# Kernel optimization log

Measured on AMD Instinct MI355X. Metric: run time of the kernel, lower is better.

The kernel has to match this reference:

```python
import jax, jax.numpy as jnp
import numpy as np
import math

D_MODEL = 1024
N_HEADS = 16
D_HEAD = D_MODEL // N_HEADS
WINDOW_LEN = 128
DILATION = 4
SEQ = 3072
BATCH = 1


def setup_inputs() -> dict:
    key = jax.random.key(0)
    ks = jax.random.split(key, 10)
    def xavier(k, shape):
        fan_out, fan_in = shape
        lim = math.sqrt(6.0 / (fan_in + fan_out))
        return jax.random.uniform(k, shape, jnp.float32, -lim, lim)
    return {
        "x": jax.random.normal(ks[0], (SEQ, BATCH, D_MODEL), jnp.float32),
        "beta": 0.1 * jax.random.normal(ks[1], (N_HEADS,), jnp.float32),
        "Wq": xavier(ks[2], (D_MODEL, D_MODEL)),
        "bq": jnp.zeros((D_MODEL,), jnp.float32),
        "Wk": xavier(ks[3], (D_MODEL, D_MODEL)),
        "bk": jnp.zeros((D_MODEL,), jnp.float32),
        "Wv": xavier(ks[4], (D_MODEL, D_MODEL)),
        "bv": jnp.zeros((D_MODEL,), jnp.float32),
        "Wo": xavier(ks[5], (D_MODEL, D_MODEL)),
        "bo": jnp.zeros((D_MODEL,), jnp.float32),
    }


def _causal_windowed_bias(seq_len):
    # allowed iff 0 <= (i-j), (i-j)//dilation < window_len, (i-j) % dilation == 0
    idx = jnp.arange(seq_len)
    diff = idx[:, None] - idx[None, :]
    allowed = (diff >= 0) & (diff // DILATION < WINDOW_LEN) & (diff % DILATION == 0)
    return jnp.where(allowed, 0.0, -jnp.inf).astype(jnp.float32)  # [S, S]


def reference(x, beta, Wq, bq, Wk, bk, Wv, bv, Wo, bo):
    s, b, d = x.shape
    # projections: nn.Linear => x @ W.T + b
    def split_heads(t):  # [s, b, h*dh] -> [b, h, s, dh]
        return t.reshape(s, b, N_HEADS, D_HEAD).transpose(1, 2, 0, 3)
    q = split_heads(x @ Wq.T + bq)
    k = split_heads(x @ Wk.T + bk)
    v = split_heads(x @ Wv.T + bv)
    # beta scaling folded into q, attention uses scale=1.0
    q = q / (math.sqrt(D_HEAD) * jnp.exp(beta)[None, :, None, None])
    bias = _causal_windowed_bias(s)  # [S, S]
    scores = jnp.einsum('bhsd,bhtd->bhst', q, k) + bias
    attn = jax.nn.softmax(scores, axis=-1)
    ctx = jnp.einsum('bhst,bhtd->bhsd', attn, v)  # [b, h, s, dh]
    ctx = ctx.transpose(2, 0, 1, 3).reshape(s, b, d)  # [s, b, d_model]
    return ctx @ Wo.T + bo
```

## Files before the change

### kernel.cpp

```cpp
#include <hip/hip_runtime.h>
#include <math.h>

#define SEQ   3072
#define DM    1024
#define NH    16
#define DH    64
#define WIN   128
#define DIL   4
#define TSUB  768

typedef __attribute__((ext_vector_type(8))) short    short8;
typedef __attribute__((ext_vector_type(8))) _Float16 half8;
typedef __attribute__((ext_vector_type(4))) float    floatx4;

__device__ __forceinline__ float bf2f(unsigned short u) {
    return __uint_as_float(((unsigned)u) << 16);
}
__device__ __forceinline__ unsigned short f2bf(float f) {
    unsigned u = __float_as_uint(f);
    return (unsigned short)((u + 0x7FFFu + ((u >> 16) & 1u)) >> 16);
}
__device__ __forceinline__ unsigned short f2h(float f) {
    _Float16 h = (_Float16)f;
    return __builtin_bit_cast(unsigned short, h);
}

__device__ __forceinline__ void gload_lds16(const void* g, void* l) {
    __builtin_amdgcn_global_load_lds(
        (const __attribute__((address_space(1))) void*)g,
        (__attribute__((address_space(3))) void*)l, 16, 0, 0);
}

__global__ __launch_bounds__(256) void convert_kernel(
    const float* __restrict__ x,  const float* __restrict__ Wq,
    const float* __restrict__ Wk, const float* __restrict__ Wv,
    const float* __restrict__ Wo,
    ushort* __restrict__ xb,  ushort* __restrict__ Wqb,
    ushort* __restrict__ Wkb, ushort* __restrict__ Wvb,
    ushort* __restrict__ Wob)
{
    const float* s; ushort* d; int n;
    switch (blockIdx.y) {
        case 0: s = x;  d = xb;  n = SEQ * DM; break;
        case 1: s = Wq; d = Wqb; n = DM * DM;  break;
        case 2: s = Wk; d = Wkb; n = DM * DM;  break;
        case 3: s = Wv; d = Wvb; n = DM * DM;  break;
        default: s = Wo; d = Wob; n = DM * DM; break;
    }
    int i = (blockIdx.x * 256 + threadIdx.x) * 4;
    if (i >= n) return;
    float4 v = *(const float4*)&s[i];
    ushort4 o = { f2bf(v.x), f2bf(v.y), f2bf(v.z), f2bf(v.w) };
    *(ushort4*)&d[i] = o;
}

struct QkvSmem {
    ushort As[2][128][64];
    ushort Bs[2][64][64];
};

template<bool QSCALE>
__device__ __forceinline__ void gemm_qkv_body(QkvSmem& sm,
                                              const ushort* __restrict__ A,
                                              const ushort* __restrict__ W,
                                              const float* __restrict__ bias,
                                              const float* __restrict__ beta,
                                              ushort* __restrict__ C,
                                              int bx, int by)
{
    const int tid  = threadIdx.x;
    const int lane = tid & 63, w = tid >> 6;
    const int ln15 = lane & 15, quad = lane >> 4;
    const int wm = w >> 1, wn = w & 1;

    const int rl = lane >> 3, cl = lane & 7;
    const ushort* aRow[4];
#pragma unroll
    for (int i = 0; i < 4; ++i) {
        int row   = w * 32 + 8 * i + rl;
        int chunk = cl ^ ((row >> 1) & 7);
        aRow[i] = A + (size_t)(by * 128 + row) * DM + chunk * 8;
    }
    const ushort* bRow[2];
#pragma unroll
    for (int i = 0; i < 2; ++i) {
        int row   = w * 16 + 8 * i + rl;
        int chunk = cl ^ ((row >> 1) & 7);
        bRow[i] = W + (size_t)(bx * 64 + row) * DM + chunk * 8;
    }

    const floatx4 zero = {0.f, 0.f, 0.f, 0.f};
    floatx4 acc[4][2];
#pragma unroll
    for (int i = 0; i < 4; ++i)
#pragma unroll
        for (int j = 0; j < 2; ++j) acc[i][j] = zero;

#pragma unroll
    for (int i = 0; i < 4; ++i) gload_lds16(aRow[i], &sm.As[0][w * 32 + 8 * i][0]);
#pragma unroll
    for (int i = 0; i < 2; ++i) gload_lds16(bRow[i], &sm.Bs[0][w * 16 + 8 * i][0]);
    __syncthreads();

    const int rf = (ln15 >> 1) & 7;
#pragma unroll 2
    for (int t = 0; t < 16; ++t) {
        const int cur = t & 1, nxt = cur ^ 1;
        if (t < 15) {
            const int ko = (t + 1) * 64;
#pragma unroll
            for (int i = 0; i < 4; ++i) gload_lds16(aRow[i] + ko, &sm.As[nxt][w * 32 + 8 * i][0]);
#pragma unroll
            for (int i = 0; i < 2; ++i) gload_lds16(bRow[i] + ko, &sm.Bs[nxt][w * 16 + 8 * i][0]);
        }
#pragma unroll
        for (int s = 0; s < 2; ++s) {
            short8 af[4], bf[2];
#pragma unroll
            for (int i = 0; i < 4; ++i)
                af[i] = *(const short8*)&sm.As[cur][wm * 64 + i * 16 + ln15][((s * 4 + quad) ^ rf) * 8];
#pragma unroll
            for (int j = 0; j < 2; ++j)
                bf[j] = *(const short8*)&sm.Bs[cur][wn * 32 + j * 16 + ln15][((s * 4 + quad) ^ rf) * 8];
#pragma unroll
            for (int i = 0; i < 4; ++i)
#pragma unroll
                for (int j = 0; j < 2; ++j)
                    acc[i][j] = __builtin_amdgcn_mfma_f32_16x16x32_bf16(af[i], bf[j], acc[i][j], 0, 0, 0);
        }
        __syncthreads();
    }

#pragma unroll
    for (int j = 0; j < 2; ++j) {
        const int col = bx * 64 + wn * 32 + j * 16 + ln15;
        const float b = bias[col];
        const float scale = QSCALE ? 0.125f * __expf(-beta[col >> 6]) : 1.0f;
#pragma unroll
        for (int i = 0; i < 4; ++i) {
            const int row0 = by * 128 + wm * 64 + i * 16 + quad * 4;
#pragma unroll
            for (int rg = 0; rg < 4; ++rg) {
                float vv = (acc[i][j][rg] + b) * scale;
                C[(size_t)(row0 + rg) * DM + col] = f2bf(vv);
            }
        }
    }
}

__global__ __launch_bounds__(256, 3) void qkv_kernel(
    const ushort* __restrict__ xb,
    const ushort* __restrict__ Wqb, const float* __restrict__ bq,
    const ushort* __restrict__ Wkb, const float* __restrict__ bk,
    const ushort* __restrict__ Wvb, const float* __restrict__ bv,
    const float* __restrict__ beta,
    ushort* __restrict__ q, ushort* __restrict__ k, ushort* __restrict__ v)
{
    __shared__ QkvSmem sm;
    const int z = blockIdx.z;
    const ushort* W = (z == 0) ? Wqb : (z == 1) ? Wkb : Wvb;
    const float*  b = (z == 0) ? bq  : (z == 1) ? bk  : bv;
    ushort*       C = (z == 0) ? q   : (z == 1) ? k   : v;
    if (z == 0)
        gemm_qkv_body<true >(sm, xb, W, b, beta, C, blockIdx.x, blockIdx.y);
    else
        gemm_qkv_body<false>(sm, xb, W, b, nullptr, C, blockIdx.x, blockIdx.y);
}

__global__ __launch_bounds__(256, 3) void out_kernel(
    const ushort* __restrict__ ctxb, const ushort* __restrict__ Wob,
    const float* __restrict__ bo, float* __restrict__ out)
{
    __shared__ ushort As[2][64][64];
    __shared__ ushort Bs[2][64][64];

    const int tid  = threadIdx.x;
    const int lane = tid & 63, w = tid >> 6;
    const int ln15 = lane & 15, quad = lane >> 4;
    const int wm = w >> 1, wn = w & 1;
    const int bx = blockIdx.x, by = blockIdx.y;

    const int rl = lane >> 3, cl = lane & 7;
    const ushort* aRow[2]; const ushort* bRow[2];
#pragma unroll
    for (int i = 0; i < 2; ++i) {
        int row   = w * 16 + 8 * i + rl;
        int chunk = cl ^ ((row >> 1) & 7);
        aRow[i] = ctxb + (size_t)(by * 64 + row) * DM + chunk * 8;
        bRow[i] = Wob  + (size_t)(bx * 64 + row) * DM + chunk * 8;
    }

    const floatx4 zero = {0.f, 0.f, 0.f, 0.f};
    floatx4 acc[2][2];
#pragma unroll
    for (int i = 0; i < 2; ++i)
#pragma unroll
        for (int j = 0; j < 2; ++j) acc[i][j] = zero;

#pragma unroll
    for (int i = 0; i < 2; ++i) {
        gload_lds16(aRow[i], &As[0][w * 16 + 8 * i][0]);
        gload_lds16(bRow[i], &Bs[0][w * 16 + 8 * i][0]);
    }
    __syncthreads();

    const int rf = (ln15 >> 1) & 7;
#pragma unroll 2
    for (int t = 0; t < 16; ++t) {
        const int cur = t & 1, nxt = cur ^ 1;
        if (t < 15) {
            const int ko = (t + 1) * 64;
#pragma unroll
            for (int i = 0; i < 2; ++i) {
                gload_lds16(aRow[i] + ko, &As[nxt][w * 16 + 8 * i][0]);
                gload_lds16(bRow[i] + ko, &Bs[nxt][w * 16 + 8 * i][0]);
            }
        }
#pragma unroll
        for (int s = 0; s < 2; ++s) {
            short8 af[2], bf[2];
#pragma unroll
            for (int i = 0; i < 2; ++i)
                af[i] = *(const short8*)&As[cur][wm * 32 + i * 16 + ln15][((s * 4 + quad) ^ rf) * 8];
#pragma unroll
            for (int j = 0; j < 2; ++j)
                bf[j] = *(const short8*)&Bs[cur][wn * 32 + j * 16 + ln15][((s * 4 + quad) ^ rf) * 8];
#pragma unroll
            for (int i = 0; i < 2; ++i)
#pragma unroll
                for (int j = 0; j < 2; ++j)
                    acc[i][j] = __builtin_amdgcn_mfma_f32_16x16x32_bf16(af[i], bf[j], acc[i][j], 0, 0, 0);
        }
        __syncthreads();
    }

#pragma unroll
    for (int j = 0; j < 2; ++j) {
        const int col = bx * 64 + wn * 32 + j * 16 + ln15;
        const float b = bo[col];
#pragma unroll
        for (int i = 0; i < 2; ++i) {
            const int row0 = by * 64 + wm * 32 + i * 16 + quad * 4;
#pragma unroll
            for (int rg = 0; rg < 4; ++rg)
                out[(size_t)(row0 + rg) * DM + col] = acc[i][j][rg] + b;
        }
    }
}

struct AttnSmem {
    union {
        ushort Ks[192 * 64];
        ushort Vt[6 * 4 * 64 * 8];
    } u;
    float S[32][195];
    float Rsum[32];
};

__global__ __launch_bounds__(256) void attn_kernel(
    const ushort* __restrict__ q, const ushort* __restrict__ k,
    const ushort* __restrict__ v, ushort* __restrict__ ctx)
{
    __shared__ AttnSmem sm;

    const int tid  = threadIdx.x;
    const int lane = tid & 63, w = tid >> 6;
    const int ln15 = lane & 15, quad = lane >> 4;
    const int t0   = blockIdx.x * 32;
    const int r    = blockIdx.y;
    const int h    = blockIdx.z;
    const int hoff = h * DH;

    {
        const int kr = lane >> 3;
        const int swz = ((lane & 7) ^ kr) * 8;
#pragma unroll
        for (int ci = w * 6; ci < w * 6 + 6; ++ci) {
            int key = ci * 8 + kr;
            long grow = 4L * (t0 - 160 + key) + r;
            gload_lds16(k + grow * DM + hoff + swz, &sm.u.Ks[ci * 512]);
        }
    }

    const int qt = w >> 1;
    short8 qf0, qf1;
    {
        int qrow = qt * 16 + ln15;
        const ushort* gq = q + (4L * (t0 + qrow) + r) * DM + hoff + quad * 8;
        qf0 = *(const short8*)gq;
        qf1 = *(const short8*)(gq + 32);
    }

    short8 vreg[6];
#pragma unroll
    for (int it = 0; it < 6; ++it) {
        int idx = it * 256 + tid;
        int key = idx >> 3, d0 = (idx & 7) * 8;
        long grow = 4L * (t0 - 160 + key) + r;
        vreg[it] = *(const short8*)(v + grow * DM + hoff + d0);
    }

    __syncthreads();

    {
        const floatx4 zero = {0.f, 0.f, 0.f, 0.f};
        const int kt0 = (w & 1) * 6;
        const int lb  = ln15 & 7;
#pragma unroll
        for (int kk2 = 0; kk2 < 6; ++kk2) {
            const int kt  = kt0 + kk2;
            const int key = kt * 16 + ln15;
            short8 b0 = *(const short8*)&sm.u.Ks[key * 64 + ((quad ^ lb) << 3)];
            short8 b1 = *(const short8*)&sm.u.Ks[key * 64 + (((4 + quad) ^ lb) << 3)];
            floatx4 acc = zero;
            acc = __builtin_amdgcn_mfma_f32_16x16x32_bf16(qf0, b0, acc, 0, 0, 0);
            acc = __builtin_amdgcn_mfma_f32_16x16x32_bf16(qf1, b1, acc, 0, 0, 0);
            const int tp = t0 - 160 + key;
#pragma unroll
            for (int rg = 0; rg < 4; ++rg) {
                int qrow = qt * 16 + quad * 4 + rg;
                int tq = t0 + qrow;
                bool ok = (tp >= 0) && (tp <= tq) && (tp > tq - WIN);
                sm.S[qrow][key] = ok ? acc[rg] : -1e30f;
            }
        }
    }

    __syncthreads();

#pragma unroll
    for (int it = 0; it < 6; ++it) {
        int idx = it * 256 + tid;
        int key = idx >> 3, d0 = (idx & 7) * 8;
        int kc = key >> 5, qd = (key >> 3) & 3, jj = key & 7;
        short8 sv = vreg[it];
#pragma unroll
        for (int u = 0; u < 8; ++u) {
            int dim = d0 + u, dt = dim >> 4, ln = dim & 15;
            sm.u.Vt[(kc * 4 + dt) * 512 + (qd * 16 + ln) * 8 + jj] =
                f2h(bf2f((unsigned short)sv[u]));
        }
    }

    {
        const int sq = tid >> 3, part = tid & 7;
        float m = -1e30f;
#pragma unroll
        for (int j = 0; j < 24; ++j) m = fmaxf(m, sm.S[sq][part + 8 * j]);
#pragma unroll
        for (int o = 1; o < 8; o <<= 1) m = fmaxf(m, __shfl_xor(m, o));
        float sum = 0.f;
#pragma unroll
        for (int j = 0; j < 24; ++j) {
            int ks = part + 8 * j;
            float e = __expf(sm.S[sq][ks] - m);
            sm.S[sq][ks] = e;
            sum += e;
        }
#pragma unroll
        for (int o = 1; o < 8; o <<= 1) sum += __shfl_xor(sum, o);
        if (part == 0) sm.Rsum[sq] = 1.0f / sum;
    }

    __syncthreads();

    {
        const floatx4 zero = {0.f, 0.f, 0.f, 0.f};
        const int qtp = w & 1, dh = w >> 1;
        floatx4 o0 = zero, o1 = zero;
#pragma unroll
        for (int kc = 0; kc < 6; ++kc) {
            const float* ps = &sm.S[qtp * 16 + ln15][kc * 32 + quad * 8];
            half8 pa;
#pragma unroll
            for (int u = 0; u < 8; ++u) pa[u] = (_Float16)ps[u];
            half8 vb0 = *(const half8*)&sm.u.Vt[(kc * 4 + dh * 2 + 0) * 512 + lane * 8];
            half8 vb1 = *(const half8*)&sm.u.Vt[(kc * 4 + dh * 2 + 1) * 512 + lane * 8];
            o0 = __builtin_amdgcn_mfma_f32_16x16x32_f16(pa, vb0, o0, 0, 0, 0);
            o1 = __builtin_amdgcn_mfma_f32_16x16x32_f16(pa, vb1, o1, 0, 0, 0);
        }
#pragma unroll
        for (int rg = 0; rg < 4; ++rg) {
            int qrow = qtp * 16 + quad * 4 + rg;
            float rs = sm.Rsum[qrow];
            long orow = 4L * (t0 + qrow) + r;
            ushort* cp = ctx + orow * DM + hoff + dh * 32 + ln15;
            cp[0]  = f2bf(o0[rg] * rs);
            cp[16] = f2bf(o1[rg] * rs);
        }
    }
}

extern "C" void kernel_launch(void* const* d_in, const int* in_sizes, int n_in,
                              void* d_out, int out_size, void* d_ws, size_t ws_size,
                              hipStream_t stream)
{
    const float* x    = (const float*)d_in[0];
    const float* beta = (const float*)d_in[1];
    const float* Wq   = (const float*)d_in[2];
    const float* bq   = (const float*)d_in[3];
    const float* Wk   = (const float*)d_in[4];
    const float* bk   = (const float*)d_in[5];
    const float* Wv   = (const float*)d_in[6];
    const float* bv   = (const float*)d_in[7];
    const float* Wo   = (const float*)d_in[8];
    const float* bo   = (const float*)d_in[9];

    ushort* qb   = (ushort*)d_ws;
    ushort* kb   = qb   + (size_t)SEQ * DM;
    ushort* vb   = kb   + (size_t)SEQ * DM;
    ushort* ctxb = vb   + (size_t)SEQ * DM;
    ushort* xb   = ctxb + (size_t)SEQ * DM;
    ushort* Wqb  = xb   + (size_t)SEQ * DM;
    ushort* Wkb  = Wqb  + (size_t)DM * DM;
    ushort* Wvb  = Wkb  + (size_t)DM * DM;
    ushort* Wob  = Wvb  + (size_t)DM * DM;
    float*  out  = (float*)d_out;

    dim3 gcv(SEQ * DM / 4 / 256, 5);
    convert_kernel<<<gcv, 256, 0, stream>>>(x, Wq, Wk, Wv, Wo, xb, Wqb, Wkb, Wvb, Wob);

    dim3 gqkv(DM / 64, SEQ / 128, 3);
    qkv_kernel<<<gqkv, 256, 0, stream>>>(xb, Wqb, bq, Wkb, bk, Wvb, bv, beta, qb, kb, vb);

    dim3 gattn(TSUB / 32, DIL, NH);
    attn_kernel<<<gattn, 256, 0, stream>>>(qb, kb, vb, ctxb);

    dim3 gout(DM / 64, SEQ / 64);
    out_kernel<<<gout, 256, 0, stream>>>(ctxb, Wob, bo, out);
}
```

Baseline: 165.0 us.

## Emit V as fp16 and load it via direct-to-LDS with transpose reads

The QKV GEMM now writes the V projection in fp16 instead of bf16, so the attention kernel no longer converts V elements. V is loaded straight into LDS through global_load_lds in a permuted layout, and the PV MFMA operands are fetched with ds_read_b64_tr_b16 transpose reads. This replaces the register-staged per-element bf16-to-fp16 transpose scatter into LDS. It adds inline asm with a full lgkmcnt wait and a sched barrier, which may serialize LDS reads against MFMA. The V load also now issues after the score phase instead of being prefetched early, so more of its latency may be exposed.

After: 153.1 us. -7.3%, faster.

```diff
diff --git a/kernel.cpp b/kernel.cpp
--- a/kernel.cpp
+++ b/kernel.cpp
@@ -11,6 +11,7 @@
 
 typedef __attribute__((ext_vector_type(8))) short    short8;
 typedef __attribute__((ext_vector_type(8))) _Float16 half8;
+typedef __attribute__((ext_vector_type(4))) _Float16 half4;
 typedef __attribute__((ext_vector_type(4))) float    floatx4;
 
 __device__ __forceinline__ float bf2f(unsigned short u) {
@@ -59,7 +60,7 @@
     ushort Bs[2][64][64];
 };
 
-template<bool QSCALE>
+template<bool QSCALE, bool F16OUT>
 __device__ __forceinline__ void gemm_qkv_body(QkvSmem& sm,
                                               const ushort* __restrict__ A,
                                               const ushort* __restrict__ W,
@@ -142,7 +143,7 @@
 #pragma unroll
             for (int rg = 0; rg < 4; ++rg) {
                 float vv = (acc[i][j][rg] + b) * scale;
-                C[(size_t)(row0 + rg) * DM + col] = f2bf(vv);
+                C[(size_t)(row0 + rg) * DM + col] = F16OUT ? f2h(vv) : f2bf(vv);
             }
         }
     }
@@ -162,9 +163,11 @@
     const float*  b = (z == 0) ? bq  : (z == 1) ? bk  : bv;
     ushort*       C = (z == 0) ? q   : (z == 1) ? k   : v;
     if (z == 0)
-        gemm_qkv_body<true >(sm, xb, W, b, beta, C, blockIdx.x, blockIdx.y);
+        gemm_qkv_body<true , false>(sm, xb, W, b, beta, C, blockIdx.x, blockIdx.y);
+    else if (z == 1)
+        gemm_qkv_body<false, false>(sm, xb, W, b, nullptr, C, blockIdx.x, blockIdx.y);
     else
-        gemm_qkv_body<false>(sm, xb, W, b, nullptr, C, blockIdx.x, blockIdx.y);
+        gemm_qkv_body<false, true >(sm, xb, W, b, nullptr, C, blockIdx.x, blockIdx.y);
 }
 
 __global__ __launch_bounds__(256, 3) void out_kernel(
@@ -251,7 +254,7 @@
 struct AttnSmem {
     union {
         ushort Ks[192 * 64];
-        ushort Vt[6 * 4 * 64 * 8];
+        ushort Vs[48 * 256];
     } u;
     float S[32][195];
     float Rsum[32];
@@ -289,15 +292,6 @@
         const ushort* gq = q + (4L * (t0 + qrow) + r) * DM + hoff + quad * 8;
         qf0 = *(const short8*)gq;
         qf1 = *(const short8*)(gq + 32);
-    }
-
-    short8 vreg[6];
-#pragma unroll
-    for (int it = 0; it < 6; ++it) {
-        int idx = it * 256 + tid;
-        int key = idx >> 3, d0 = (idx & 7) * 8;
-        long grow = 4L * (t0 - 160 + key) + r;
-        vreg[it] = *(const short8*)(v + grow * DM + hoff + d0);
     }
 
     __syncthreads();
@@ -328,17 +322,18 @@
 
     __syncthreads();
 
-#pragma unroll
-    for (int it = 0; it < 6; ++it) {
-        int idx = it * 256 + tid;
-        int key = idx >> 3, d0 = (idx & 7) * 8;
-        int kc = key >> 5, qd = (key >> 3) & 3, jj = key & 7;
-        short8 sv = vreg[it];
-#pragma unroll
-        for (int u = 0; u < 8; ++u) {
-            int dim = d0 + u, dt = dim >> 4, ln = dim & 15;
-            sm.u.Vt[(kc * 4 + dt) * 512 + (qd * 16 + ln) * 8 + jj] =
-                f2h(bf2f((unsigned short)sv[u]));
+    {
+#pragma unroll
+        for (int i = 0; i < 6; ++i) {
+            const int o  = w * 6 + i;
+            const int c  = o * 64 + lane;
+            const int hh = c & 1, jj = (c >> 1) & 3, qq = (c >> 3) & 3;
+            const int T  = c >> 5;
+            const int p  = T & 1, dtt = (T >> 1) & 3, kc = T >> 3;
+            const int key = kc * 32 + qq * 8 + p * 4 + jj;
+            const int dim = dtt * 16 + hh * 8;
+            long grow = 4L * (t0 - 160 + key) + r;
+            gload_lds16(v + grow * DM + hoff + dim, &sm.u.Vs[o * 512]);
         }
     }
 
@@ -368,14 +363,27 @@
         const floatx4 zero = {0.f, 0.f, 0.f, 0.f};
         const int qtp = w & 1, dh = w >> 1;
         floatx4 o0 = zero, o1 = zero;
+        const unsigned vbase =
+            (unsigned)(size_t)(__attribute__((address_space(3))) ushort*)&sm.u.Vs[0]
+            + lane * 8 + dh * 2048;
 #pragma unroll
         for (int kc = 0; kc < 6; ++kc) {
             const float* ps = &sm.S[qtp * 16 + ln15][kc * 32 + quad * 8];
             half8 pa;
 #pragma unroll
             for (int u = 0; u < 8; ++u) pa[u] = (_Float16)ps[u];
-            half8 vb0 = *(const half8*)&sm.u.Vt[(kc * 4 + dh * 2 + 0) * 512 + lane * 8];
-            half8 vb1 = *(const half8*)&sm.u.Vt[(kc * 4 + dh * 2 + 1) * 512 + lane * 8];
+            half4 a0, a1, b0, b1;
+            asm volatile(
+                "ds_read_b64_tr_b16 %0, %4\n\t"
+                "ds_read_b64_tr_b16 %1, %4 offset:512\n\t"
+                "ds_read_b64_tr_b16 %2, %4 offset:1024\n\t"
+                "ds_read_b64_tr_b16 %3, %4 offset:1536\n\t"
+                "s_waitcnt lgkmcnt(0)"
+                : "=&v"(a0), "=&v"(a1), "=&v"(b0), "=&v"(b1)
+                : "v"(vbase + kc * 4096));
+            __builtin_amdgcn_sched_barrier(0);
+            half8 vb0 = __builtin_shufflevector(a0, a1, 0, 1, 2, 3, 4, 5, 6, 7);
+            half8 vb1 = __builtin_shufflevector(b0, b1, 0, 1, 2, 3, 4, 5, 6, 7);
             o0 = __builtin_amdgcn_mfma_f32_16x16x32_f16(pa, vb0, o0, 0, 0, 0);
             o1 = __builtin_amdgcn_mfma_f32_16x16x32_f16(pa, vb1, o1, 0, 0, 0);
         }
```
